# Kernel tuning notes

Measured on AMD Instinct MI355X. Metric: run time of the kernel, lower is better.

The kernel has to match this reference:

```python
import jax, jax.numpy as jnp
import numpy as np

B, S, D, H, DFF = 4, 2048, 2048, 16, 8192
DH = D // H
THETA = 10000.0
EPS = 1e-5


def rmsnorm(x, g):
    return x * jax.lax.rsqrt(jnp.mean(x * x, axis=-1, keepdims=True) + EPS) * g


def rope(x, pos):
    # x: [B, H, S, DH]; rotate interleaved even/odd pairs
    half = DH // 2
    inv_freq = THETA ** (-(jnp.arange(half, dtype=jnp.float32) * 2.0) / DH)  # [half]
    ang = pos.astype(jnp.float32)[:, None] * inv_freq  # [S, half]
    cos, sin = jnp.cos(ang), jnp.sin(ang)
    x1, x2 = x[..., 0::2], x[..., 1::2]
    r1 = x1 * cos - x2 * sin
    r2 = x1 * sin + x2 * cos
    return jnp.stack([r1, r2], axis=-1).reshape(x.shape)


def setup_inputs() -> dict:
    key = jax.random.key(0)
    ks = jax.random.split(key, 12)
    s = 0.02
    return {
        "x": jax.random.normal(ks[0], (B, S, D), dtype=jnp.float32),
        "attention_mask": jnp.ones((S, S), dtype=bool),
        "wq": jax.random.normal(ks[1], (D, D), dtype=jnp.float32) * s,
        "wk": jax.random.normal(ks[2], (D, D), dtype=jnp.float32) * s,
        "wv": jax.random.normal(ks[3], (D, D), dtype=jnp.float32) * s,
        "wo": jax.random.normal(ks[4], (D, D), dtype=jnp.float32) * s,
        "w1": jax.random.normal(ks[5], (DFF, D), dtype=jnp.float32) * s,
        "w2": jax.random.normal(ks[6], (D, DFF), dtype=jnp.float32) * s,
        "w3": jax.random.normal(ks[7], (DFF, D), dtype=jnp.float32) * s,
        "g1": jnp.ones((D,), dtype=jnp.float32),
        "g2": jnp.ones((D,), dtype=jnp.float32),
    }


def reference(x, attention_mask, wq, wk, wv, wo, w1, w2, w3, g1, g2):
    pos = jnp.arange(x.shape[-2])
    # pre-norm attention
    h = rmsnorm(x, g1)
    q = (h @ wq.T).reshape(B, S, H, DH).transpose(0, 2, 1, 3)
    k = (h @ wk.T).reshape(B, S, H, DH).transpose(0, 2, 1, 3)
    v = (h @ wv.T).reshape(B, S, H, DH).transpose(0, 2, 1, 3)
    q = rope(q, pos)
    k = rope(k, pos)
    scores = jnp.einsum("bhqd,bhkd->bhqk", q, k) / np.float32(np.sqrt(DH))
    scores = jnp.where(attention_mask, scores, jnp.float32(-1e9))
    attn = jax.nn.softmax(scores, axis=-1)
    o = jnp.einsum("bhqk,bhkd->bhqd", attn, v)
    o = o.transpose(0, 2, 1, 3).reshape(B, S, D) @ wo.T
    x = x + o
    # pre-norm SwiGLU FFN
    h2 = rmsnorm(x, g2)
    ffn = (jax.nn.silu(h2 @ w1.T) * (h2 @ w3.T)) @ w2.T
    return x + ffn
```

## Files before the change

### kernel.cpp

```cpp
#include <hip/hip_runtime.h>
#include <cstdint>
#include <cstddef>

#define B_   4
#define S_   2048
#define D_   2048
#define H_   16
#define DH_  128
#define DFF_ 8192
#define LOG2E 1.4426950408889634f

typedef __bf16 bf16_t;
typedef __bf16 bf16x4 __attribute__((ext_vector_type(4)));
typedef __bf16 bf16x8 __attribute__((ext_vector_type(8)));
typedef float  f32x4  __attribute__((ext_vector_type(4)));

#define MFMA16 __builtin_amdgcn_mfma_f32_16x16x32_bf16

__device__ __forceinline__ void glds16(const void* g, void* l) {
  __builtin_amdgcn_global_load_lds((__attribute__((address_space(1))) void*)g,
                                   (__attribute__((address_space(3))) void*)l,
                                   16, 0, 0);
}

__global__ __launch_bounds__(256) void cvt_kernel(const float* __restrict__ in,
                                                  bf16_t* __restrict__ out, int n8) {
  int i = blockIdx.x * 256 + threadIdx.x;
  if (i >= n8) return;
  const float4* p4 = (const float4*)in;
  float4 a = p4[2 * (size_t)i];
  float4 b = p4[2 * (size_t)i + 1];
  bf16x8 o;
  o[0] = (bf16_t)a.x; o[1] = (bf16_t)a.y; o[2] = (bf16_t)a.z; o[3] = (bf16_t)a.w;
  o[4] = (bf16_t)b.x; o[5] = (bf16_t)b.y; o[6] = (bf16_t)b.z; o[7] = (bf16_t)b.w;
  ((bf16x8*)out)[i] = o;
}

__global__ __launch_bounds__(256) void rmsnorm_kernel(const float* __restrict__ x,
                                                      const float* __restrict__ g,
                                                      bf16_t* __restrict__ out) {
  const int row = blockIdx.x, tid = threadIdx.x;
  const float* xr = x + (size_t)row * D_;
  float4 a = ((const float4*)xr)[tid * 2];
  float4 b = ((const float4*)xr)[tid * 2 + 1];
  float ss = a.x*a.x + a.y*a.y + a.z*a.z + a.w*a.w
           + b.x*b.x + b.y*b.y + b.z*b.z + b.w*b.w;
#pragma unroll
  for (int m = 1; m < 64; m <<= 1) ss += __shfl_xor(ss, m);
  __shared__ float red[4];
  if ((tid & 63) == 0) red[tid >> 6] = ss;
  __syncthreads();
  float tot = red[0] + red[1] + red[2] + red[3];
  float rms = rsqrtf(tot * (1.0f / D_) + 1e-5f);
  float4 ga = ((const float4*)g)[tid * 2];
  float4 gb = ((const float4*)g)[tid * 2 + 1];
  bf16x8 o;
  o[0] = (bf16_t)(a.x * rms * ga.x); o[1] = (bf16_t)(a.y * rms * ga.y);
  o[2] = (bf16_t)(a.z * rms * ga.z); o[3] = (bf16_t)(a.w * rms * ga.w);
  o[4] = (bf16_t)(b.x * rms * gb.x); o[5] = (bf16_t)(b.y * rms * gb.y);
  o[6] = (bf16_t)(b.z * rms * gb.z); o[7] = (bf16_t)(b.w * rms * gb.w);
  ((bf16x8*)out)[(size_t)row * 256 + tid] = o;
}

template <int EPI>
__global__ __launch_bounds__(512, 4) void gemm256h(const bf16_t* __restrict__ A,
                                                   const bf16_t* __restrict__ W,
                                                   const float* __restrict__ addf,
                                                   const bf16_t* __restrict__ addb,
                                                   bf16_t* __restrict__ outb,
                                                   bf16_t* __restrict__ outb2,
                                                   bf16_t* __restrict__ outb3,
                                                   float* __restrict__ outf,
                                                   int M, int N, int K) {
  __shared__ char ldsb[49152];
  const int tid = threadIdx.x;
  const int wid = tid >> 6, l = tid & 63, l15 = l & 15, lg = l >> 4;
  const int wm = wid >> 2, wn = wid & 3;

  const int nwg = gridDim.x;
  int wg = (int)blockIdx.x;
  wg = (wg & 7) * (nwg >> 3) + (wg >> 3);
  const int ntm = M >> 7;
  const int wide = 4 * ntm;
  const int grp = wg / wide;
  const int rem = wg % wide;
  const int m0 = (rem >> 2) << 7;
  const int n0 = ((grp << 2) + (rem & 3)) << 8;

  f32x4 acc[4][4];
  const f32x4 z4 = {0.f, 0.f, 0.f, 0.f};
#pragma unroll
  for (int i = 0; i < 4; i++)
#pragma unroll
    for (int j = 0; j < 4; j++) acc[i][j] = z4;

  const int o0 = tid * 16;
  const int srow = o0 >> 7;
  const int ssw = ((o0 & 127) ^ ((srow & 7) << 4)) >> 1;
  const bf16_t* Asrc = A + (size_t)(m0 + srow) * K + ssw;
  const bf16_t* Wsrc = W + (size_t)(n0 + srow) * K + ssw;
  const int rsw = (l15 & 7) << 4;
  const int acol0 = (lg * 16) ^ rsw;
  const int acol1 = (64 + lg * 16) ^ rsw;

  const int NT = K >> 6;
  for (int t = 0; t < NT; t++) {
    const bf16_t* as = Asrc + (size_t)t * 64;
    glds16(as, ldsb + o0);
    glds16(as + 64 * (size_t)K, ldsb + 8192 + o0);
    const bf16_t* ws = Wsrc + (size_t)t * 64;
    glds16(ws, ldsb + 16384 + o0);
    glds16(ws + 64 * (size_t)K, ldsb + 24576 + o0);
    glds16(ws + 128 * (size_t)K, ldsb + 32768 + o0);
    glds16(ws + 192 * (size_t)K, ldsb + 40960 + o0);
    asm volatile("s_waitcnt vmcnt(0)" ::: "memory");
    __builtin_amdgcn_s_barrier();
    __builtin_amdgcn_sched_barrier(0);
    bf16x8 af[4][2];
#pragma unroll
    for (int fi = 0; fi < 4; fi++) {
      const char* p = ldsb + (wm * 64 + fi * 16 + l15) * 128;
      af[fi][0] = *(const bf16x8*)(p + acol0);
      af[fi][1] = *(const bf16x8*)(p + acol1);
    }
    __builtin_amdgcn_s_setprio(1);
#pragma unroll
    for (int n = 0; n < 4; n++) {
      const char* p = ldsb + 16384 + (wn * 64 + n * 16 + l15) * 128;
      bf16x8 b0 = *(const bf16x8*)(p + acol0);
      bf16x8 b1 = *(const bf16x8*)(p + acol1);
#pragma unroll
      for (int m = 0; m < 4; m++) {
        acc[m][n] = MFMA16(af[m][0], b0, acc[m][n], 0, 0, 0);
        acc[m][n] = MFMA16(af[m][1], b1, acc[m][n], 0, 0, 0);
      }
    }
    __builtin_amdgcn_s_setprio(0);
    __builtin_amdgcn_sched_barrier(0);
    __builtin_amdgcn_s_barrier();
  }

#pragma unroll
  for (int m = 0; m < 4; m++) {
    const int gr = m0 + wm * 64 + m * 16 + lg * 4;
#pragma unroll
    for (int n = 0; n < 4; n++) {
      const int gc = n0 + wn * 64 + n * 16 + l15;
      if constexpr (EPI == 4) {
        const int seg = gc >> 11;
        const int gcl = gc & 2047;
        if (seg < 2) {
          bf16_t* o = seg ? outb2 : outb;
#pragma unroll
          for (int r = 0; r < 4; r++)
            o[(size_t)(gr + r) * D_ + gcl] = (bf16_t)acc[m][n][r];
        } else {
          const int bb = gr >> 11, ss = gr & 2047;
          bf16x4 pk;
#pragma unroll
          for (int r = 0; r < 4; r++) pk[r] = (bf16_t)acc[m][n][r];
          *(bf16x4*)(outb3 + ((size_t)bb * D_ + gcl) * S_ + ss) = pk;
        }
      } else {
#pragma unroll
        for (int r = 0; r < 4; r++) {
          size_t idx = (size_t)(gr + r) * N + gc;
          if constexpr (EPI == 0) {
            outb[idx] = (bf16_t)acc[m][n][r];
          } else if constexpr (EPI == 1) {
            outf[idx] = acc[m][n][r] + addf[idx];
          } else {
            float a1v = (float)addb[idx];
            outb[idx] = (bf16_t)(a1v / (1.0f + expf(-a1v)) * acc[m][n][r]);
          }
        }
      }
    }
  }
}

template <int EPI>
__global__ __launch_bounds__(512, 4) void gemm256h2(const bf16_t* __restrict__ A,
                                                    const bf16_t* __restrict__ W,
                                                    const bf16_t* __restrict__ addb,
                                                    bf16_t* __restrict__ outb,
                                                    int M, int N, int K) {
  __shared__ char ldsb[49152];
  const int tid = threadIdx.x;
  const int wid = tid >> 6, l = tid & 63, l15 = l & 15, lg = l >> 4;
  const int wm = wid >> 2, wn = wid & 3;

  const int nwg = gridDim.x;
  int wg = (int)blockIdx.x;
  wg = (wg & 7) * (nwg >> 3) + (wg >> 3);
  const int ntm = M >> 7;
  const int wide = 4 * ntm;
  const int grp = wg / wide;
  const int rem = wg % wide;
  const int m0 = (rem >> 2) << 7;
  const int n0 = ((grp << 2) + (rem & 3)) << 8;

  f32x4 acc[4][4];
  const f32x4 z4 = {0.f, 0.f, 0.f, 0.f};
#pragma unroll
  for (int i = 0; i < 4; i++)
#pragma unroll
    for (int j = 0; j < 4; j++) acc[i][j] = z4;

  const int o0 = tid * 16;
  const int srow = o0 >> 6;
  const int ssw = ((o0 & 63) ^ ((srow & 3) << 4)) >> 1;
  const bf16_t* Asrc = A + (size_t)(m0 + srow) * K + ssw;
  const bf16_t* Wsrc = W + (size_t)(n0 + srow) * K + ssw;
  const int rsw = (l15 & 3) << 4;
  const int acol = (lg * 16) ^ rsw;

#define H2_STAGE(d, kt)                                                       \
  do {                                                                        \
    const bf16_t* a_ = Asrc + (size_t)(kt) * 32;                              \
    glds16(a_, ldsb + (d) * 24576 + o0);                                      \
    const bf16_t* w_ = Wsrc + (size_t)(kt) * 32;                              \
    glds16(w_, ldsb + (d) * 24576 + 8192 + o0);                               \
    glds16(w_ + 128 * (size_t)K, ldsb + (d) * 24576 + 16384 + o0);            \
  } while (0)

  const int NT = K >> 5;
  H2_STAGE(0, 0);
  H2_STAGE(1, 1);

  for (int t = 0; t < NT; t++) {
    const int d = t & 1;
    if (t + 1 < NT) asm volatile("s_waitcnt vmcnt(3)" ::: "memory");
    else            asm volatile("s_waitcnt vmcnt(0)" ::: "memory");
    __builtin_amdgcn_s_barrier();
    __builtin_amdgcn_sched_barrier(0);
    const char* ab = ldsb + d * 24576;
    bf16x8 af[4];
#pragma unroll
    for (int m = 0; m < 4; m++)
      af[m] = *(const bf16x8*)(ab + (wm * 64 + m * 16 + l15) * 64 + acol);
    __builtin_amdgcn_s_setprio(1);
#pragma unroll
    for (int n = 0; n < 4; n++) {
      bf16x8 bf = *(const bf16x8*)(ab + 8192 + (wn * 64 + n * 16 + l15) * 64 + acol);
#pragma unroll
      for (int m = 0; m < 4; m++)
        acc[m][n] = MFMA16(af[m], bf, acc[m][n], 0, 0, 0);
    }
    __builtin_amdgcn_s_setprio(0);
    __builtin_amdgcn_sched_barrier(0);
    __builtin_amdgcn_s_barrier();
    if (t + 2 < NT) H2_STAGE(d, t + 2);
  }

#pragma unroll
  for (int m = 0; m < 4; m++) {
    const int gr = m0 + wm * 64 + m * 16 + lg * 4;
#pragma unroll
    for (int n = 0; n < 4; n++) {
      const int gc = n0 + wn * 64 + n * 16 + l15;
#pragma unroll
      for (int r = 0; r < 4; r++) {
        size_t idx = (size_t)(gr + r) * N + gc;
        if constexpr (EPI == 0) {
          outb[idx] = (bf16_t)acc[m][n][r];
        } else {
          float a1v = (float)addb[idx];
          outb[idx] = (bf16_t)(a1v / (1.0f + expf(-a1v)) * acc[m][n][r]);
        }
      }
    }
  }
#undef H2_STAGE
}

__global__ __launch_bounds__(256) void rope_kernel(bf16_t* __restrict__ buf) {
  size_t i = (size_t)blockIdx.x * 256 + threadIdx.x;
  int pi = (int)(i & 63);
  size_t rh = i >> 6;
  int srow = (int)((rh / H_) % S_);
  float inv = expf((float)pi * (-9.210340371976184f / 64.0f));
  float ang = (float)srow * inv;
  float c = cosf(ang), sn = sinf(ang);
  bf16_t* p = buf + i * 2;
  float x1 = (float)p[0], x2 = (float)p[1];
  p[0] = (bf16_t)(x1 * c - x2 * sn);
  p[1] = (bf16_t)(x1 * sn + x2 * c);
}

__global__ __launch_bounds__(256) void attn_kernel(const bf16_t* __restrict__ Q,
                                                   const bf16_t* __restrict__ Kb,
                                                   const bf16_t* __restrict__ Vt,
                                                   bf16_t* __restrict__ O) {
  const int qt = blockIdx.x, h = blockIdx.y, b = blockIdx.z;
  const int tid = threadIdx.x;
  const int wid = tid >> 6, l = tid & 63, l15 = l & 15, lg = l >> 4;

  __shared__ bf16_t Klds[64 * 128];
  __shared__ bf16_t Vlds[128 * 64];
  __shared__ bf16_t Plds[4][16 * 72];

  const int q0 = qt * 64 + wid * 16;
  const f32x4 z4 = {0.f, 0.f, 0.f, 0.f};
  const float SCL = 0.08838834764831845f * LOG2E;

  bf16x8 qf[4];
  {
    const bf16_t* qp = Q + ((size_t)(b * S_ + q0 + l15)) * D_ + h * DH_ + lg * 8;
#pragma unroll
    for (int kk = 0; kk < 4; kk++) qf[kk] = *(const bf16x8*)(qp + kk * 32);
  }
  f32x4 of[8];
#pragma unroll
  for (int f = 0; f < 8; f++) of[f] = z4;
  float m_run = -1e30f, l_run = 0.f;

  const int o0 = tid * 16;
  const int krow0 = o0 >> 8;
  const int scol = ((o0 & 255) ^ ((krow0 & 7) << 4)) >> 1;
  const int vrow0 = o0 >> 7;
  const int vcol = ((o0 & 127) ^ ((vrow0 & 7) << 4)) >> 1;

  const size_t bh_off = ((size_t)b * S_) * D_ + (size_t)h * DH_;
  const bf16_t* vtbase = Vt + ((size_t)b * D_ + h * DH_) * S_;

  for (int kv0 = 0; kv0 < S_; kv0 += 64) {
    const bf16_t* kbase = Kb + bh_off + (size_t)kv0 * D_;
#pragma unroll
    for (int s = 0; s < 4; s++)
      glds16(kbase + (size_t)(krow0 + 16 * s) * D_ + scol,
             (char*)Klds + s * 4096 + wid * 1024);
#pragma unroll
    for (int s = 0; s < 4; s++)
      glds16(vtbase + (size_t)(vrow0 + 32 * s) * S_ + kv0 + vcol,
             (char*)Vlds + s * 4096 + wid * 1024);
    __syncthreads();

    f32x4 st[4];
#pragma unroll
    for (int c = 0; c < 4; c++) {
      st[c] = z4;
      const int row = c * 16 + l15;
      const char* kr = (const char*)Klds + row * 256;
      const int sw = (row & 7) << 4;
#pragma unroll
      for (int kk = 0; kk < 4; kk++) {
        bf16x8 kf = *(const bf16x8*)(kr + ((kk * 64 + lg * 16) ^ sw));
        st[c] = MFMA16(kf, qf[kk], st[c], 0, 0, 0);
      }
    }

    float s[16];
#pragma unroll
    for (int c = 0; c < 4; c++)
#pragma unroll
      for (int r = 0; r < 4; r++) s[c * 4 + r] = st[c][r] * SCL;
    float pm = s[0];
#pragma unroll
    for (int i = 1; i < 16; i++) pm = fmaxf(pm, s[i]);
    pm = fmaxf(pm, __shfl_xor(pm, 16));
    pm = fmaxf(pm, __shfl_xor(pm, 32));
    if (!__all(pm - m_run <= 8.0f)) {
      float mnew = fmaxf(m_run, pm);
      float alpha = exp2f(m_run - mnew);
      float aq[4];
#pragma unroll
      for (int r = 0; r < 4; r++) aq[r] = __shfl(alpha, lg * 4 + r);
#pragma unroll
      for (int f = 0; f < 8; f++)
#pragma unroll
        for (int r = 0; r < 4; r++) of[f][r] *= aq[r];
      l_run *= alpha;
      m_run = mnew;
    }
    float p[16], ts = 0.f;
#pragma unroll
    for (int i = 0; i < 16; i++) { p[i] = exp2f(s[i] - m_run); ts += p[i]; }
    ts += __shfl_xor(ts, 16);
    ts += __shfl_xor(ts, 32);
    l_run += ts;

    bf16_t* pw = &Plds[wid][0];
#pragma unroll
    for (int c = 0; c < 4; c++)
#pragma unroll
      for (int r = 0; r < 4; r++)
        pw[l15 * 72 + c * 16 + lg * 4 + r] = (bf16_t)p[c * 4 + r];
    asm volatile("s_waitcnt lgkmcnt(0)" ::: "memory");
    bf16x8 pa0 = *(const bf16x8*)(pw + l15 * 72 + lg * 8);
    bf16x8 pa1 = *(const bf16x8*)(pw + l15 * 72 + 32 + lg * 8);
#pragma unroll
    for (int f = 0; f < 8; f++) {
      const int row = 16 * f + l15;
      const char* vr = (const char*)Vlds + row * 128;
      const int sw = (row & 7) << 4;
      bf16x8 bv0 = *(const bf16x8*)(vr + ((lg * 16) ^ sw));
      bf16x8 bv1 = *(const bf16x8*)(vr + ((64 + lg * 16) ^ sw));
      of[f] = MFMA16(pa0, bv0, of[f], 0, 0, 0);
      of[f] = MFMA16(pa1, bv1, of[f], 0, 0, 0);
    }
    __syncthreads();
  }

  float inv[4];
#pragma unroll
  for (int r = 0; r < 4; r++) inv[r] = 1.0f / __shfl(l_run, lg * 4 + r);
#pragma unroll
  for (int f = 0; f < 8; f++)
#pragma unroll
    for (int r = 0; r < 4; r++)
      O[((size_t)(b * S_ + q0 + lg * 4 + r)) * D_ + h * DH_ + 16 * f + l15] =
          (bf16_t)(of[f][r] * inv[r]);
}

extern "C" void kernel_launch(void* const* d_in, const int* in_sizes, int n_in,
                              void* d_out, int out_size, void* d_ws, size_t ws_size,
                              hipStream_t stream) {
  const float* x  = (const float*)d_in[0];
  const float* wq = (const float*)d_in[2];
  const float* wk = (const float*)d_in[3];
  const float* wv = (const float*)d_in[4];
  const float* wo = (const float*)d_in[5];
  const float* w1 = (const float*)d_in[6];
  const float* w2 = (const float*)d_in[7];
  const float* w3 = (const float*)d_in[8];
  const float* g1 = (const float*)d_in[9];
  const float* g2 = (const float*)d_in[10];
  float* out = (float*)d_out;

  const size_t ND = (size_t)D_ * D_;
  const size_t NF = (size_t)DFF_ * D_;
  const size_t SLOT = NF * 2;
  char* base = (char*)d_ws;
  bf16_t* wslot = (bf16_t*)(base);
  bf16_t* h1    = (bf16_t*)(base + 1 * SLOT);
  bf16_t* qb    = (bf16_t*)(base + 2 * SLOT);
  bf16_t* kb    = (bf16_t*)(base + 3 * SLOT);
  bf16_t* vt    = (bf16_t*)(base + 4 * SLOT);
  bf16_t* ob    = (bf16_t*)(base + 5 * SLOT);
  bf16_t* h2    = h1;
  bf16_t* g     = qb;
  float*  x1    = out;

  auto cvt = [&](const float* in, bf16_t* o, size_t n) {
    int n8 = (int)(n / 8);
    cvt_kernel<<<(n8 + 255) / 256, 256, 0, stream>>>(in, o, n8);
  };

  rmsnorm_kernel<<<B_ * S_, 256, 0, stream>>>(x, g1, h1);

  cvt(wq, wslot, ND);
  cvt(wk, wslot + ND, ND);
  cvt(wv, wslot + 2 * ND, ND);
  const int gqkv3 = (8192 / 128) * (6144 / 256);
  gemm256h<4><<<gqkv3, 512, 0, stream>>>(h1, wslot, nullptr, nullptr,
                                         qb, kb, vt, nullptr, 8192, 6144, 2048);

  rope_kernel<<<(B_ * S_ * H_ * 64) / 256, 256, 0, stream>>>(qb);
  rope_kernel<<<(B_ * S_ * H_ * 64) / 256, 256, 0, stream>>>(kb);

  dim3 ga(S_ / 64, H_, B_);
  attn_kernel<<<ga, 256, 0, stream>>>(qb, kb, vt, ob);

  const int gd = (8192 / 128) * (2048 / 256);
  cvt(wo, wslot, ND);
  gemm256h<1><<<gd, 512, 0, stream>>>(ob, wslot, x, nullptr,
                                      nullptr, nullptr, nullptr, x1, 8192, 2048, 2048);

  rmsnorm_kernel<<<B_ * S_, 256, 0, stream>>>(x1, g2, h2);

  const int gffh = (8192 / 128) * (8192 / 256);
  cvt(w1, wslot, NF);
  gemm256h2<0><<<gffh, 512, 0, stream>>>(h2, wslot, nullptr, g, 8192, 8192, 2048);

  cvt(w3, wslot, NF);
  gemm256h2<2><<<gffh, 512, 0, stream>>>(h2, wslot, g, g, 8192, 8192, 2048);

  cvt(w2, wslot, NF);
  gemm256h<1><<<gd, 512, 0, stream>>>(g, wslot, x1, nullptr,
                                      nullptr, nullptr, nullptr, x1, 8192, 2048, 8192);
}
```

Before: 1.457 ms.

## Replace FFN up/gate GEMM with 4-wave 256x128 tile kernel, vectorize P stores

The two FFN GEMMs (w1 and w3) now use a new kernel with 4 waves per block, each owning a 128x64 sub-tile. The block tile changes from 128x256 to 256x128, and the K step grows from 32 to 64 with a wider 128-byte LDS swizzle. The double-buffered async prefetch is gone: each iteration loads its tile, waits on vmcnt(0), then computes, so memory and compute no longer overlap inside a block. Separately, the attention kernel writes softmax probabilities to LDS as packed bf16x4 instead of scalar stores.

```diff
diff --git a/kernel.cpp b/kernel.cpp
--- a/kernel.cpp
+++ b/kernel.cpp
@@ -180,82 +180,82 @@
 }
 
 template <int EPI>
-__global__ __launch_bounds__(512, 4) void gemm256h2(const bf16_t* __restrict__ A,
-                                                    const bf16_t* __restrict__ W,
-                                                    const bf16_t* __restrict__ addb,
-                                                    bf16_t* __restrict__ outb,
-                                                    int M, int N, int K) {
+__global__ __launch_bounds__(256, 2) void gemm4w(const bf16_t* __restrict__ A,
+                                                 const bf16_t* __restrict__ W,
+                                                 const bf16_t* __restrict__ addb,
+                                                 bf16_t* __restrict__ outb,
+                                                 int M, int N, int K) {
   __shared__ char ldsb[49152];
   const int tid = threadIdx.x;
   const int wid = tid >> 6, l = tid & 63, l15 = l & 15, lg = l >> 4;
-  const int wm = wid >> 2, wn = wid & 3;
+  const int wm = wid >> 1, wn = wid & 1;
 
   const int nwg = gridDim.x;
   int wg = (int)blockIdx.x;
   wg = (wg & 7) * (nwg >> 3) + (wg >> 3);
-  const int ntm = M >> 7;
+  const int ntm = M >> 8;
   const int wide = 4 * ntm;
   const int grp = wg / wide;
   const int rem = wg % wide;
-  const int m0 = (rem >> 2) << 7;
-  const int n0 = ((grp << 2) + (rem & 3)) << 8;
-
-  f32x4 acc[4][4];
+  const int m0 = (rem >> 2) << 8;
+  const int n0 = ((grp << 2) + (rem & 3)) << 7;
+
+  f32x4 acc[8][4];
   const f32x4 z4 = {0.f, 0.f, 0.f, 0.f};
 #pragma unroll
-  for (int i = 0; i < 4; i++)
+  for (int i = 0; i < 8; i++)
 #pragma unroll
     for (int j = 0; j < 4; j++) acc[i][j] = z4;
 
   const int o0 = tid * 16;
-  const int srow = o0 >> 6;
-  const int ssw = ((o0 & 63) ^ ((srow & 3) << 4)) >> 1;
+  const int srow = o0 >> 7;
+  const int ssw = ((o0 & 127) ^ ((srow & 7) << 4)) >> 1;
   const bf16_t* Asrc = A + (size_t)(m0 + srow) * K + ssw;
   const bf16_t* Wsrc = W + (size_t)(n0 + srow) * K + ssw;
-  const int rsw = (l15 & 3) << 4;
-  const int acol = (lg * 16) ^ rsw;
-
-#define H2_STAGE(d, kt)                                                       \
-  do {                                                                        \
-    const bf16_t* a_ = Asrc + (size_t)(kt) * 32;                              \
-    glds16(a_, ldsb + (d) * 24576 + o0);                                      \
-    const bf16_t* w_ = Wsrc + (size_t)(kt) * 32;                              \
-    glds16(w_, ldsb + (d) * 24576 + 8192 + o0);                               \
-    glds16(w_ + 128 * (size_t)K, ldsb + (d) * 24576 + 16384 + o0);            \
-  } while (0)
-
-  const int NT = K >> 5;
-  H2_STAGE(0, 0);
-  H2_STAGE(1, 1);
-
+  const int rsw = (l15 & 7) << 4;
+  const int acol0 = (lg * 16) ^ rsw;
+  const int acol1 = (64 + lg * 16) ^ rsw;
+
+  const int NT = K >> 6;
   for (int t = 0; t < NT; t++) {
-    const int d = t & 1;
-    if (t + 1 < NT) asm volatile("s_waitcnt vmcnt(3)" ::: "memory");
-    else            asm volatile("s_waitcnt vmcnt(0)" ::: "memory");
+    const bf16_t* as = Asrc + (size_t)t * 64;
+#pragma unroll
+    for (int p = 0; p < 8; p++)
+      glds16(as + (size_t)(32 * p) * K, ldsb + p * 4096 + o0);
+    const bf16_t* ws = Wsrc + (size_t)t * 64;
+#pragma unroll
+    for (int p = 0; p < 4; p++)
+      glds16(ws + (size_t)(32 * p) * K, ldsb + 32768 + p * 4096 + o0);
+    asm volatile("s_waitcnt vmcnt(0)" ::: "memory");
     __builtin_amdgcn_s_barrier();
     __builtin_amdgcn_sched_barrier(0);
-    const char* ab = ldsb + d * 24576;
-    bf16x8 af[4];
-#pragma unroll
-    for (int m = 0; m < 4; m++)
-      af[m] = *(const bf16x8*)(ab + (wm * 64 + m * 16 + l15) * 64 + acol);
+    bf16x8 af[8][2];
+#pragma unroll
+    for (int m = 0; m < 8; m++) {
+      const char* p = ldsb + (wm * 128 + m * 16 + l15) * 128;
+      af[m][0] = *(const bf16x8*)(p + acol0);
+      af[m][1] = *(const bf16x8*)(p + acol1);
+    }
     __builtin_amdgcn_s_setprio(1);
 #pragma unroll
     for (int n = 0; n < 4; n++) {
-      bf16x8 bf = *(const bf16x8*)(ab + 8192 + (wn * 64 + n * 16 + l15) * 64 + acol);
-#pragma unroll
-      for (int m = 0; m < 4; m++)
-        acc[m][n] = MFMA16(af[m], bf, acc[m][n], 0, 0, 0);
+      const char* p = ldsb + 32768 + (wn * 64 + n * 16 + l15) * 128;
+      bf16x8 b0 = *(const bf16x8*)(p + acol0);
+      bf16x8 b1 = *(const bf16x8*)(p + acol1);
+#pragma unroll
+      for (int m = 0; m < 8; m++) {
+        acc[m][n] = MFMA16(af[m][0], b0, acc[m][n], 0, 0, 0);
+        acc[m][n] = MFMA16(af[m][1], b1, acc[m][n], 0, 0, 0);
+      }
     }
     __builtin_amdgcn_s_setprio(0);
     __builtin_amdgcn_sched_barrier(0);
     __builtin_amdgcn_s_barrier();
-    if (t + 2 < NT) H2_STAGE(d, t + 2);
-  }
-
-#pragma unroll
-  for (int m = 0; m < 4; m++) {
-    const int gr = m0 + wm * 64 + m * 16 + lg * 4;
+  }
+
+#pragma unroll
+  for (int m = 0; m < 8; m++) {
+    const int gr = m0 + wm * 128 + m * 16 + lg * 4;
 #pragma unroll
     for (int n = 0; n < 4; n++) {
       const int gc = n0 + wn * 64 + n * 16 + l15;
@@ -271,7 +271,6 @@
       }
     }
   }
-#undef H2_STAGE
 }
 
 __global__ __launch_bounds__(256) void rope_kernel(bf16_t* __restrict__ buf) {
@@ -382,10 +381,12 @@
 
     bf16_t* pw = &Plds[wid][0];
 #pragma unroll
-    for (int c = 0; c < 4; c++)
-#pragma unroll
-      for (int r = 0; r < 4; r++)
-        pw[l15 * 72 + c * 16 + lg * 4 + r] = (bf16_t)p[c * 4 + r];
+    for (int c = 0; c < 4; c++) {
+      bf16x4 pk;
+#pragma unroll
+      for (int r = 0; r < 4; r++) pk[r] = (bf16_t)p[c * 4 + r];
+      *(bf16x4*)(pw + l15 * 72 + c * 16 + lg * 4) = pk;
+    }
     asm volatile("s_waitcnt lgkmcnt(0)" ::: "memory");
     bf16x8 pa0 = *(const bf16x8*)(pw + l15 * 72 + lg * 8);
     bf16x8 pa1 = *(const bf16x8*)(pw + l15 * 72 + 32 + lg * 8);
@@ -469,12 +470,12 @@
 
   rmsnorm_kernel<<<B_ * S_, 256, 0, stream>>>(x1, g2, h2);
 
-  const int gffh = (8192 / 128) * (8192 / 256);
+  const int g4w = (8192 / 256) * (8192 / 128);
   cvt(w1, wslot, NF);
-  gemm256h2<0><<<gffh, 512, 0, stream>>>(h2, wslot, nullptr, g, 8192, 8192, 2048);
+  gemm4w<0><<<g4w, 256, 0, stream>>>(h2, wslot, nullptr, g, 8192, 8192, 2048);
 
   cvt(w3, wslot, NF);
-  gemm256h2<2><<<gffh, 512, 0, stream>>>(h2, wslot, g, g, 8192, 8192, 2048);
+  gemm4w<2><<<g4w, 256, 0, stream>>>(h2, wslot, g, g, 8192, 8192, 2048);
 
   cvt(w2, wslot, NF);
   gemm256h<1><<<gd, 512, 0, stream>>>(g, wslot, x1, nullptr,
```

After: 1.416 ms. -2.8%, faster.
